# Kernel tuning notes

Measured on AMD Instinct MI355X. Metric: run time of the kernel, lower is better.

## Reference

```python
import jax, jax.numpy as jnp
import numpy as np

N_NODES = 50000
N_EDGES = 1200000
IN_FEATS = 64
OUT_FEATS = 64
NEG_SLOPE = 0.01  # F.leaky_relu default


def setup_inputs() -> dict:
    key = jax.random.key(0)
    k1, k2, k3, k4, k5, k6 = jax.random.split(key, 6)
    feature = jax.random.normal(k1, (N_NODES, IN_FEATS), dtype=jnp.float32)
    attn_w = jax.random.normal(k2, (2 * IN_FEATS, 1), dtype=jnp.float32) * 0.1
    lin_w = jax.random.normal(k3, (OUT_FEATS, 2 * IN_FEATS), dtype=jnp.float32) * 0.1
    lin_b = jax.random.normal(k4, (OUT_FEATS,), dtype=jnp.float32) * 0.1
    src = jax.random.randint(k5, (N_EDGES,), 0, N_NODES, dtype=jnp.int32)
    dst = jax.random.randint(k6, (N_EDGES,), 0, N_NODES, dtype=jnp.int32)
    return {"feature": feature, "attn_w": attn_w, "lin_w": lin_w,
            "lin_b": lin_b, "src": src, "dst": dst}


def reference(feature, attn_w, lin_w, lin_b, src, dst):
    N = feature.shape[0]
    # edge attention: leaky_relu(attn_fc([h_src, h_dst]))
    # split attn weight to avoid materializing the [E, 2*in] concat
    a_src, a_dst = attn_w[:IN_FEATS, 0], attn_w[IN_FEATS:, 0]
    e = jax.nn.leaky_relu(feature[src] @ a_src + feature[dst] @ a_dst,
                          negative_slope=NEG_SLOPE)  # [E]
    # segment softmax over incoming edges of each destination node
    emax = jax.ops.segment_max(e, dst, num_segments=N)
    emax = jnp.where(jnp.isfinite(emax), emax, 0.0)  # guard empty segments
    ex = jnp.exp(e - emax[dst])                       # [E]
    denom = jax.ops.segment_sum(ex, dst, num_segments=N)          # [N]
    num = jax.ops.segment_sum(ex[:, None] * feature[src], dst,
                              num_segments=N)                      # [N, in]
    hm = jnp.where(denom[:, None] > 0, num / denom[:, None], 0.0)
    # node apply: relu(Linear([h, hm]))
    h = jnp.concatenate([feature, hm], axis=1) @ lin_w.T + lin_b
    return jax.nn.relu(h)
```

## Files before the change

kernel.cpp:

```cpp
#include <hip/hip_runtime.h>
#include <math.h>

#define N_NODES 50000
#define N_EDGES 1200000
#define F 64
#define CAP 49
#define OVF_MAX 1024
#define NBIN 782
#define BSTR 16
#define CAP_BIN 2304
#define TILE 8192
#define NTILE ((N_EDGES + TILE - 1) / TILE)
#define XSTR 72

typedef __attribute__((ext_vector_type(8))) short short8;
typedef __attribute__((ext_vector_type(4))) float v4f;


__device__ __forceinline__ unsigned short f32_to_bf16_rne(float f) {
    unsigned u = __float_as_uint(f);
    return (unsigned short)((u + 0x7FFFu + ((u >> 16) & 1u)) >> 16);
}
__device__ __forceinline__ float bf16_to_f32(unsigned short u) {
    return __uint_as_float(((unsigned)u) << 16);
}

__global__ void k_prep(const float* __restrict__ feature,
                       const float* __restrict__ attn_w,
                       float* __restrict__ s, float* __restrict__ dd,
                       int* __restrict__ bin_cnt, int* __restrict__ ovf_cnt,
                       unsigned short* __restrict__ fb) {
    int gid = blockIdx.x * blockDim.x + threadIdx.x;
    if (gid < NBIN * BSTR) bin_cnt[gid] = 0;
    if (gid == NBIN * BSTR) *ovf_cnt = 0;
    int wave = gid >> 6;
    int lane = threadIdx.x & 63;
    if (wave >= N_NODES) return;
    float f = feature[wave * F + lane];
    fb[wave * F + lane] = f32_to_bf16_rne(f);
    float sv = f * attn_w[lane];
    float dv = f * attn_w[F + lane];
    #pragma unroll
    for (int o = 32; o > 0; o >>= 1) {
        sv += __shfl_down(sv, o, 64);
        dv += __shfl_down(dv, o, 64);
    }
    if (lane == 0) {
        s[wave] = sv;
        dd[wave] = dv;
    }
}

__global__ __launch_bounds__(256) void k_bin(
        const int* __restrict__ src, const int* __restrict__ dst,
        int* __restrict__ bin_cnt, unsigned* __restrict__ binned) {
    __shared__ unsigned ord[TILE];
    __shared__ int cnt_l[NBIN], off_l[NBIN], cur_l[NBIN], base_g[NBIN];
    __shared__ int buf[256];
    int t = threadIdx.x;
    int e0 = blockIdx.x * TILE;
    int ecnt = N_EDGES - e0; if (ecnt > TILE) ecnt = TILE;
    for (int i = t; i < NBIN; i += 256) cnt_l[i] = 0;
    __syncthreads();
    int n4 = ecnt >> 2;
    const int4* s4p = (const int4*)src + (e0 >> 2);
    const int4* d4p = (const int4*)dst + (e0 >> 2);
    unsigned pk[32];
    int ng = 0;
    #pragma unroll
    for (int k = 0; k < 8; k++) {
        int c = t + k * 256;
        if (c < n4) {
            int4 d4 = d4p[c];
            int4 s4 = s4p[c];
            pk[4 * k + 0] = (((unsigned)d4.x) << 16) | (unsigned)s4.x;
            pk[4 * k + 1] = (((unsigned)d4.y) << 16) | (unsigned)s4.y;
            pk[4 * k + 2] = (((unsigned)d4.z) << 16) | (unsigned)s4.z;
            pk[4 * k + 3] = (((unsigned)d4.w) << 16) | (unsigned)s4.w;
            atomicAdd(&cnt_l[pk[4 * k + 0] >> 22], 1);
            atomicAdd(&cnt_l[pk[4 * k + 1] >> 22], 1);
            atomicAdd(&cnt_l[pk[4 * k + 2] >> 22], 1);
            atomicAdd(&cnt_l[pk[4 * k + 3] >> 22], 1);
            ng = k + 1;
        }
    }
    __syncthreads();
    int c0[4];
    int sum = 0;
    #pragma unroll
    for (int j = 0; j < 4; j++) {
        int idx = t * 4 + j;
        c0[j] = (idx < NBIN) ? cnt_l[idx] : 0;
        sum += c0[j];
    }
    buf[t] = sum;
    __syncthreads();
    #pragma unroll
    for (int d = 1; d < 256; d <<= 1) {
        int x = (t >= d) ? buf[t - d] : 0;
        __syncthreads();
        buf[t] += x;
        __syncthreads();
    }
    int excl = buf[t] - sum;
    #pragma unroll
    for (int j = 0; j < 4; j++) {
        int idx = t * 4 + j;
        if (idx < NBIN) {
            off_l[idx] = excl;
            cur_l[idx] = excl;
            base_g[idx] = atomicAdd(&bin_cnt[idx * BSTR], c0[j]);
        }
        excl += c0[j];
    }
    __syncthreads();
    for (int k = 0; k < ng; k++) {
        #pragma unroll
        for (int u = 0; u < 4; u++) {
            unsigned v = pk[4 * k + u];
            int r = atomicAdd(&cur_l[v >> 22], 1);
            ord[r] = v;
        }
    }
    __syncthreads();
    for (int i = t; i < ecnt; i += 256) {
        unsigned v = ord[i];
        int b = v >> 22;
        int pos = base_g[b] + (i - off_l[b]);
        if (pos < CAP_BIN) binned[(size_t)b * CAP_BIN + pos] = v;
    }
}

__global__ __launch_bounds__(256, 4) void k_fused(
        const unsigned* __restrict__ binned, const int* __restrict__ bin_cnt,
        int* __restrict__ cnt, unsigned short* __restrict__ bucket,
        int* __restrict__ ovf_cnt, unsigned* __restrict__ ovf,
        const float* __restrict__ s, const float* __restrict__ dd,
        const unsigned short* __restrict__ fb,
        const float* __restrict__ lin_w, const float* __restrict__ lin_b,
        float* __restrict__ out) {
    __shared__ int cnt_l[64];
    __shared__ unsigned short buck_l[64 * CAP];
    __shared__ unsigned short Wl[64 * 136];
    __shared__ __align__(16) unsigned short xl[4][16][XSTR];
    int t = threadIdx.x;
    int wid = t >> 6, lane = t & 63;
    int bin = blockIdx.x;
    int n0 = bin << 6;
    int nn = N_NODES - n0; if (nn > 64) nn = 64;
    for (int i = t; i < 64 * 128; i += 256)
        Wl[(i >> 7) * 136 + (i & 127)] = f32_to_bf16_rne(lin_w[i]);
    if (t < 64) cnt_l[t] = 0;
    __syncthreads();
    int E = bin_cnt[bin * BSTR];
    if (E > CAP_BIN) E = CAP_BIN;
    const unsigned* be = binned + (size_t)bin * CAP_BIN;
    for (int i = t; i < E; i += 256) {
        unsigned v = be[i];
        int local = (v >> 16) & 63;
        int sid = (int)(v & 0xFFFFu);
        int r = atomicAdd(&cnt_l[local], 1);
        if (r < CAP) {
            buck_l[local * CAP + r] = (unsigned short)sid;
        } else {
            int o = atomicAdd(ovf_cnt, 1);
            if (o < OVF_MAX)
                ovf[o] = ((unsigned)(n0 + local) << 16) | (unsigned)sid;
        }
    }
    __syncthreads();
    if (t < nn) {
        cnt[n0 + t] = cnt_l[t];
        if (cnt_l[t] > CAP) {
            for (int k2 = 0; k2 < CAP; k2++)
                bucket[(size_t)(n0 + t) * CAP + k2] = buck_l[t * CAP + k2];
        }
    }
    __syncthreads();
    const ushort4* f4 = (const ushort4*)fb;
    for (int j = 0; j < 16; j++) {
        int local = wid * 16 + j;
        if (local >= nn) break;
        int deg = cnt_l[local];
        if (deg == 0 || deg > CAP) {
            if (lane < 16) {
                ushort4 z = {0, 0, 0, 0};
                *(ushort4*)&xl[wid][j][lane * 4] = z;
            }
            continue;
        }
        int si = 0;
        float ev = -1e30f;
        if (lane < deg) {
            si = (int)buck_l[local * CAP + lane];
            float v = s[si] + dd[n0 + local];
            ev = v > 0.0f ? v : 0.01f * v;
        }
        float m = ev;
        #pragma unroll
        for (int o = 32; o > 0; o >>= 1)
            m = fmaxf(m, __shfl_xor(m, o, 64));
        float p = (lane < deg) ? __expf(ev - m) : 0.0f;
        float l = p;
        #pragma unroll
        for (int o = 32; o > 0; o >>= 1)
            l += __shfl_xor(l, o, 64);
        p *= __builtin_amdgcn_rcpf(l);
        int grp = lane >> 4;
        int c16 = lane & 15;
        ushort4 fv0[8], fv1[8];
        #pragma unroll
        for (int u = 0; u < 8; u++) {
            int sk = __shfl(si, u * 4 + grp, 64);
            fv0[u] = f4[sk * 16 + c16];
        }
        bool two = deg > 32;
        if (two) {
            #pragma unroll
            for (int u = 0; u < 8; u++) {
                int sk = __shfl(si, 32 + u * 4 + grp, 64);
                fv1[u] = f4[sk * 16 + c16];
            }
        }
        float a0 = 0.0f, a1 = 0.0f, a2 = 0.0f, a3 = 0.0f;
        #pragma unroll
        for (int u = 0; u < 8; u++) {
            float pw = __shfl(p, u * 4 + grp, 64);
            a0 = fmaf(pw, bf16_to_f32(fv0[u].x), a0);
            a1 = fmaf(pw, bf16_to_f32(fv0[u].y), a1);
            a2 = fmaf(pw, bf16_to_f32(fv0[u].z), a2);
            a3 = fmaf(pw, bf16_to_f32(fv0[u].w), a3);
        }
        if (two) {
            #pragma unroll
            for (int u = 0; u < 8; u++) {
                float pw = __shfl(p, 32 + u * 4 + grp, 64);
                a0 = fmaf(pw, bf16_to_f32(fv1[u].x), a0);
                a1 = fmaf(pw, bf16_to_f32(fv1[u].y), a1);
                a2 = fmaf(pw, bf16_to_f32(fv1[u].z), a2);
                a3 = fmaf(pw, bf16_to_f32(fv1[u].w), a3);
            }
        }
        a0 += __shfl_xor(a0, 16, 64); a0 += __shfl_xor(a0, 32, 64);
        a1 += __shfl_xor(a1, 16, 64); a1 += __shfl_xor(a1, 32, 64);
        a2 += __shfl_xor(a2, 16, 64); a2 += __shfl_xor(a2, 32, 64);
        a3 += __shfl_xor(a3, 16, 64); a3 += __shfl_xor(a3, 32, 64);
        if (lane < 16) {
            ushort4 st;
            st.x = f32_to_bf16_rne(a0);
            st.y = f32_to_bf16_rne(a1);
            st.z = f32_to_bf16_rne(a2);
            st.w = f32_to_bf16_rne(a3);
            *(ushort4*)&xl[wid][j][c16 * 4] = st;
        }
    }
    int n0w = n0 + wid * 16;
    if (n0w >= N_NODES) return;
    int m = lane & 15, quad = lane >> 4;
    short8 afr[4];
    #pragma unroll
    for (int ks = 0; ks < 2; ks++) {
        int kb = ks * 32 + quad * 8;
        afr[ks] = *(const short8*)&fb[(size_t)(n0w + m) * F + kb];
    }
    #pragma unroll
    for (int ks = 2; ks < 4; ks++) {
        int kb = (ks - 2) * 32 + quad * 8;
        afr[ks] = *(const short8*)&xl[wid][m][kb];
    }
    #pragma unroll
    for (int nt = 0; nt < 4; nt++) {
        v4f acc = {0.0f, 0.0f, 0.0f, 0.0f};
        #pragma unroll
        for (int ks = 0; ks < 4; ks++) {
            int kb = ks * 32 + quad * 8;
            short8 b = *(const short8*)&Wl[(nt * 16 + m) * 136 + kb];
            acc = __builtin_amdgcn_mfma_f32_16x16x32_bf16(afr[ks], b, acc,
                                                          0, 0, 0);
        }
        int colo = nt * 16 + m;
        float bias = lin_b[colo];
        #pragma unroll
        for (int r = 0; r < 4; r++) {
            int row = quad * 4 + r;
            float v = acc[r] + bias;
            out[(size_t)(n0w + row) * F + colo] = fmaxf(v, 0.0f);
        }
    }
}

__global__ __launch_bounds__(256) void k_cleanup(
        const unsigned short* __restrict__ bucket,
        const int* __restrict__ cnt,
        const int* __restrict__ ovf_cnt, const unsigned int* __restrict__ ovf,
        const float* __restrict__ s, const float* __restrict__ dd,
        const float* __restrict__ feature,
        const float* __restrict__ lin_w, const float* __restrict__ lin_b,
        float* __restrict__ out) {
    int M = *ovf_cnt;
    if (M > OVF_MAX) M = OVF_MAX;
    if (M == 0) return;
    __shared__ float Wl[64 * 129];
    __shared__ int list[128];
    __shared__ int nlist;
    __shared__ unsigned short edg[4][256];
    __shared__ float xc[4][128];
    int t = threadIdx.x;
    for (int i = t; i < 64 * 128; i += 256)
        Wl[(i >> 7) * 129 + (i & 127)] = lin_w[i];
    if (t == 0) {
        nlist = 0;
        for (int i = 0; i < M; i++) {
            int d = (int)(ovf[i] >> 16);
            bool seen = false;
            for (int j = 0; j < nlist; j++) if (list[j] == d) seen = true;
            if (!seen && nlist < 128) list[nlist++] = d;
        }
    }
    __syncthreads();
    int wid = t >> 6, lane = t & 63;
    for (int idx = wid; idx < nlist; idx += 4) {
        int n = list[idx];
        int deg = cnt[n];
        if (lane < CAP) edg[wid][lane] = bucket[n * CAP + lane];
        int k2 = CAP;
        for (int base = 0; base < M; base += 64) {
            int i2 = base + lane;
            unsigned val = 0;
            bool mt = false;
            if (i2 < M) { val = ovf[i2]; mt = ((int)(val >> 16) == n); }
            unsigned long long mask = __ballot(mt);
            if (mt) {
                int pos = k2 + __popcll(mask & ((1ULL << lane) - 1ULL));
                if (pos < 256) edg[wid][pos] = (unsigned short)(val & 0xFFFFu);
            }
            k2 += __popcll(mask);
        }
        __threadfence_block();
        int nd = deg < 256 ? deg : 256;
        float m = -1e30f, l = 0.0f, acc = 0.0f;
        float dn = dd[n];
        for (int c0 = 0; c0 < nd; c0 += 64) {
            int j = c0 + lane;
            int sid = 0;
            float ev = -1e30f;
            if (j < nd) {
                sid = (int)edg[wid][j];
                float v = s[sid] + dn;
                ev = v > 0.0f ? v : 0.01f * v;
            }
            float cm = ev;
            #pragma unroll
            for (int o = 32; o > 0; o >>= 1)
                cm = fmaxf(cm, __shfl_xor(cm, o, 64));
            float np = (j < nd) ? __expf(ev - cm) : 0.0f;
            float cl = np;
            #pragma unroll
            for (int o = 32; o > 0; o >>= 1)
                cl += __shfl_xor(cl, o, 64);
            float cacc = 0.0f;
            int c = nd - c0; if (c > 64) c = 64;
            for (int k = 0; k < c; k += 16) {
                float fvv[16];
                #pragma unroll
                for (int u = 0; u < 16; u++) {
                    int sk = __builtin_amdgcn_readlane(sid, k + u);
                    fvv[u] = feature[sk * F + lane];
                }
                #pragma unroll
                for (int u = 0; u < 16; u++) {
                    float pk = __uint_as_float(
                        __builtin_amdgcn_readlane(__float_as_uint(np), k + u));
                    cacc = fmaf(pk, fvv[u], cacc);
                }
            }
            float mn = fmaxf(m, cm);
            float sc = __expf(m - mn);
            float sc2 = __expf(cm - mn);
            l = l * sc + cl * sc2;
            acc = acc * sc + cacc * sc2;
            m = mn;
        }
        float hm = acc / l;
        xc[wid][lane] = feature[n * F + lane];
        xc[wid][64 + lane] = hm;
        __threadfence_block();
        float oa = lin_b[lane];
        #pragma unroll
        for (int k = 0; k < 128; k++)
            oa += xc[wid][k] * Wl[lane * 129 + k];
        out[n * F + lane] = fmaxf(oa, 0.0f);
    }
}

extern "C" void kernel_launch(void* const* d_in, const int* in_sizes, int n_in,
                              void* d_out, int out_size, void* d_ws, size_t ws_size,
                              hipStream_t stream) {
    const float* feature = (const float*)d_in[0];
    const float* attn_w  = (const float*)d_in[1];
    const float* lin_w   = (const float*)d_in[2];
    const float* lin_b   = (const float*)d_in[3];
    const int*   src     = (const int*)d_in[4];
    const int*   dst     = (const int*)d_in[5];
    float* out = (float*)d_out;
    char* ws = (char*)d_ws;

    float*          s       = (float*)(ws);
    float*          dd      = (float*)(ws + 200000);
    int*            cnt     = (int*)  (ws + 400000);
    int*            bin_cnt = (int*)  (ws + 600000);
    int*            ovf_cnt = (int*)  (ws + 650048);
    unsigned*       ovf     = (unsigned*)(ws + 650112);
    unsigned short* bucket  = (unsigned short*)(ws + 654208);
    unsigned*       binned  = (unsigned*)(ws + 5554208);
    unsigned short* fb      = (unsigned short*)(ws + 12761120);

    k_prep<<<(N_NODES * 64) / 256, 256, 0, stream>>>(
        feature, attn_w, s, dd, bin_cnt, ovf_cnt, fb);
    k_bin<<<NTILE, 256, 0, stream>>>(src, dst, bin_cnt, binned);
    k_fused<<<NBIN, 256, 0, stream>>>(
        binned, bin_cnt, cnt, bucket, ovf_cnt, ovf, s, dd, fb,
        lin_w, lin_b, out);
    k_cleanup<<<1, 256, 0, stream>>>(
        bucket, cnt, ovf_cnt, ovf, s, dd, feature, lin_w, lin_b, out);
}
```

Baseline: 141.9 us.

## Drop softmax max-shift and stage neighbor ids/weights in LDS for vector gather

Removes the per-node wave max reduction in the segment softmax, exponentiating logits directly. The neighbor ids and normalized weights now go through padded, zeroed shared memory, so each lane reads 8 ids and 8 weights with vector loads instead of many cross-lane shuffles. The counter reset moves from k_prep to a hipMemsetAsync. Skipping the max shift risks overflow for large logits, and the memset adds an extra operation on the stream.

```diff
diff --git a/kernel.cpp b/kernel.cpp
--- a/kernel.cpp
+++ b/kernel.cpp
@@ -5,6 +5,7 @@
 #define N_EDGES 1200000
 #define F 64
 #define CAP 49
+#define BSTR2 56
 #define OVF_MAX 1024
 #define NBIN 782
 #define BSTR 16
@@ -14,6 +15,7 @@
 #define XSTR 72
 
 typedef __attribute__((ext_vector_type(8))) short short8;
+typedef __attribute__((ext_vector_type(8))) unsigned short ushort8_t;
 typedef __attribute__((ext_vector_type(4))) float v4f;
 
 
@@ -28,11 +30,8 @@
 __global__ void k_prep(const float* __restrict__ feature,
                        const float* __restrict__ attn_w,
                        float* __restrict__ s, float* __restrict__ dd,
-                       int* __restrict__ bin_cnt, int* __restrict__ ovf_cnt,
                        unsigned short* __restrict__ fb) {
     int gid = blockIdx.x * blockDim.x + threadIdx.x;
-    if (gid < NBIN * BSTR) bin_cnt[gid] = 0;
-    if (gid == NBIN * BSTR) *ovf_cnt = 0;
     int wave = gid >> 6;
     int lane = threadIdx.x & 63;
     if (wave >= N_NODES) return;
@@ -140,9 +139,10 @@
         const float* __restrict__ lin_w, const float* __restrict__ lin_b,
         float* __restrict__ out) {
     __shared__ int cnt_l[64];
-    __shared__ unsigned short buck_l[64 * CAP];
+    __shared__ __align__(16) unsigned short buck_l[64 * BSTR2];
     __shared__ unsigned short Wl[64 * 136];
     __shared__ __align__(16) unsigned short xl[4][16][XSTR];
+    __shared__ __align__(16) float p_l[4][64];
     int t = threadIdx.x;
     int wid = t >> 6, lane = t & 63;
     int bin = blockIdx.x;
@@ -151,6 +151,11 @@
     for (int i = t; i < 64 * 128; i += 256)
         Wl[(i >> 7) * 136 + (i & 127)] = f32_to_bf16_rne(lin_w[i]);
     if (t < 64) cnt_l[t] = 0;
+    {
+        uint4 z4 = {0, 0, 0, 0};
+        uint4* b4 = (uint4*)buck_l;
+        for (int i = t; i < 448; i += 256) b4[i] = z4;
+    }
     __syncthreads();
     int E = bin_cnt[bin * BSTR];
     if (E > CAP_BIN) E = CAP_BIN;
@@ -161,7 +166,7 @@
         int sid = (int)(v & 0xFFFFu);
         int r = atomicAdd(&cnt_l[local], 1);
         if (r < CAP) {
-            buck_l[local * CAP + r] = (unsigned short)sid;
+            buck_l[local * BSTR2 + r] = (unsigned short)sid;
         } else {
             int o = atomicAdd(ovf_cnt, 1);
             if (o < OVF_MAX)
@@ -173,11 +178,13 @@
         cnt[n0 + t] = cnt_l[t];
         if (cnt_l[t] > CAP) {
             for (int k2 = 0; k2 < CAP; k2++)
-                bucket[(size_t)(n0 + t) * CAP + k2] = buck_l[t * CAP + k2];
+                bucket[(size_t)(n0 + t) * CAP + k2] = buck_l[t * BSTR2 + k2];
         }
     }
     __syncthreads();
     const ushort4* f4 = (const ushort4*)fb;
+    int grp = lane >> 4;
+    int c16 = lane & 15;
     for (int j = 0; j < 16; j++) {
         int local = wid * 16 + j;
         if (local >= nn) break;
@@ -189,56 +196,35 @@
             }
             continue;
         }
-        int si = 0;
-        float ev = -1e30f;
+        float pr = 0.0f;
         if (lane < deg) {
-            si = (int)buck_l[local * CAP + lane];
+            int si = (int)buck_l[local * BSTR2 + lane];
             float v = s[si] + dd[n0 + local];
-            ev = v > 0.0f ? v : 0.01f * v;
-        }
-        float m = ev;
-        #pragma unroll
-        for (int o = 32; o > 0; o >>= 1)
-            m = fmaxf(m, __shfl_xor(m, o, 64));
-        float p = (lane < deg) ? __expf(ev - m) : 0.0f;
-        float l = p;
+            v = v > 0.0f ? v : 0.01f * v;
+            pr = __expf(v);
+        }
+        float l = pr;
         #pragma unroll
         for (int o = 32; o > 0; o >>= 1)
             l += __shfl_xor(l, o, 64);
-        p *= __builtin_amdgcn_rcpf(l);
-        int grp = lane >> 4;
-        int c16 = lane & 15;
-        ushort4 fv0[8], fv1[8];
-        #pragma unroll
-        for (int u = 0; u < 8; u++) {
-            int sk = __shfl(si, u * 4 + grp, 64);
-            fv0[u] = f4[sk * 16 + c16];
-        }
-        bool two = deg > 32;
-        if (two) {
+        p_l[wid][lane] = pr * __builtin_amdgcn_rcpf(l);
+        float a0 = 0.0f, a1 = 0.0f, a2 = 0.0f, a3 = 0.0f;
+        for (int e0 = 0; e0 < deg; e0 += 32) {
+            ushort8_t skv = *(const ushort8_t*)
+                &buck_l[local * BSTR2 + e0 + grp * 8];
+            float4 pA = *(const float4*)&p_l[wid][e0 + grp * 8];
+            float4 pB = *(const float4*)&p_l[wid][e0 + grp * 8 + 4];
+            ushort4 fv[8];
+            #pragma unroll
+            for (int u = 0; u < 8; u++)
+                fv[u] = f4[(int)skv[u] * 16 + c16];
+            float pw[8] = {pA.x, pA.y, pA.z, pA.w, pB.x, pB.y, pB.z, pB.w};
             #pragma unroll
             for (int u = 0; u < 8; u++) {
-                int sk = __shfl(si, 32 + u * 4 + grp, 64);
-                fv1[u] = f4[sk * 16 + c16];
-            }
-        }
-        float a0 = 0.0f, a1 = 0.0f, a2 = 0.0f, a3 = 0.0f;
-        #pragma unroll
-        for (int u = 0; u < 8; u++) {
-            float pw = __shfl(p, u * 4 + grp, 64);
-            a0 = fmaf(pw, bf16_to_f32(fv0[u].x), a0);
-            a1 = fmaf(pw, bf16_to_f32(fv0[u].y), a1);
-            a2 = fmaf(pw, bf16_to_f32(fv0[u].z), a2);
-            a3 = fmaf(pw, bf16_to_f32(fv0[u].w), a3);
-        }
-        if (two) {
-            #pragma unroll
-            for (int u = 0; u < 8; u++) {
-                float pw = __shfl(p, 32 + u * 4 + grp, 64);
-                a0 = fmaf(pw, bf16_to_f32(fv1[u].x), a0);
-                a1 = fmaf(pw, bf16_to_f32(fv1[u].y), a1);
-                a2 = fmaf(pw, bf16_to_f32(fv1[u].z), a2);
-                a3 = fmaf(pw, bf16_to_f32(fv1[u].w), a3);
+                a0 = fmaf(pw[u], bf16_to_f32(fv[u].x), a0);
+                a1 = fmaf(pw[u], bf16_to_f32(fv[u].y), a1);
+                a2 = fmaf(pw[u], bf16_to_f32(fv[u].z), a2);
+                a3 = fmaf(pw[u], bf16_to_f32(fv[u].w), a3);
             }
         }
         a0 += __shfl_xor(a0, 16, 64); a0 += __shfl_xor(a0, 32, 64);
@@ -415,8 +401,9 @@
     unsigned*       binned  = (unsigned*)(ws + 5554208);
     unsigned short* fb      = (unsigned short*)(ws + 12761120);
 
+    hipMemsetAsync(ws + 600000, 0, 50112, stream);
     k_prep<<<(N_NODES * 64) / 256, 256, 0, stream>>>(
-        feature, attn_w, s, dd, bin_cnt, ovf_cnt, fb);
+        feature, attn_w, s, dd, fb);
     k_bin<<<NTILE, 256, 0, stream>>>(src, dst, bin_cnt, binned);
     k_fused<<<NBIN, 256, 0, stream>>>(
         binned, bin_cnt, cnt, bucket, ovf_cnt, ovf, s, dd, fb,
```

Result: no change. 142.3 us (+0.3%).
